# Optimization experiments

Hardware: AMD Instinct MI355X
Metric: run time of the kernel (lower is better)

The kernel has to match this reference:

```python
import jax, jax.numpy as jnp
import numpy as np

H = 28; W = 28; N = H * W
P = N              # padded max persistence pairs per homology dimension
T = 32             # landscape resolution
K1, K2 = 2, 3      # K_max for the two topo layers
M0_1, M0_2 = 0.05, 0.2
LIMS = ((1.0, 28.0), (1.0, 28.0))


def _make_nbrs(h, w, conn8):
    idx = np.arange(h * w).reshape(h, w)
    offs = [(-1, 0), (1, 0), (0, -1), (0, 1)]
    if conn8:
        offs += [(-1, -1), (-1, 1), (1, -1), (1, 1)]
    nbrs = []
    for i in range(h):
        for j in range(w):
            cur = [idx[i + a, j + b] for a, b in offs if 0 <= i + a < h and 0 <= j + b < w]
            nbrs.append(np.asarray(cur, np.int64))
    return nbrs

_NBR4 = _make_nbrs(H, W, False)
_NBR8 = _make_nbrs(H, W, True)


def _h0_pairs(vals, nbrs):
    # 0-dim persistence pairs of a vertex-valued sublevel filtration (union-find, elder rule)
    order = np.argsort(vals, kind="stable")
    pos = np.empty(N, np.int64); pos[order] = np.arange(N)
    parent = np.arange(N); birth = np.arange(N)
    added = np.zeros(N, bool)
    bi = np.zeros(P, np.int32); di = np.zeros(P, np.int32)
    k = 0
    def find(x):
        r = x
        while parent[r] != r: r = parent[r]
        while parent[x] != r: parent[x], x = r, parent[x]
        return r
    for v in order:
        added[v] = True
        for u in nbrs[v]:
            if not added[u]: continue
            ru, rv = find(u), find(v)
            if ru == rv: continue
            if pos[birth[ru]] <= pos[birth[rv]]:
                lb = birth[rv]; parent[rv] = ru
            else:
                lb = birth[ru]; parent[ru] = rv
            if k < P:
                bi[k] = lb; di[k] = v; k += 1
    return bi, di


def _pers_pairs_np(x):
    # x: [M, N] -> (birth_idx, death_idx) each [M, 2, P]; padded pairs point at idx 0 (zero persistence)
    x = np.asarray(x, np.float64)
    M = x.shape[0]
    bi = np.zeros((M, 2, P), np.int32); di = np.zeros((M, 2, P), np.int32)
    for m in range(M):
        b0, d0 = _h0_pairs(x[m], _NBR4)      # H0: sublevel, 4-connectivity
        b1, d1 = _h0_pairs(-x[m], _NBR8)     # H1 by Alexander duality: H0 of superlevel, 8-connectivity
        bi[m, 0], di[m, 0] = b0, d0
        bi[m, 1], di[m, 1] = d1, b1          # H1 birth = vals[d1], death = vals[b1]
    return bi, di


def _grid_d2():
    xs = np.linspace(LIMS[0][0], LIMS[0][1], H)
    ys = np.linspace(LIMS[1][0], LIMS[1][1], W)
    gx, gy = np.meshgrid(xs, ys, indexing="ij")
    pts = np.stack([gx.ravel(), gy.ravel()], 1)              # [N, 2] grid coordinates
    d2 = ((pts[:, None, :] - pts[None, :, :]) ** 2).sum(-1)  # [N, N] squared distances
    si = np.argsort(d2, axis=1, kind="stable")
    return jnp.asarray(si), jnp.asarray(np.take_along_axis(d2, si, 1), jnp.float32)

_SORT_IDX, _D2S = _grid_d2()


def dtm(x_flat, m0):
    # weighted distance-to-measure on the pixel grid, r=2; x_flat: [M, N] positive weights
    bound = m0 * jnp.sum(x_flat, -1, keepdims=True)                        # [M, 1]
    ws = x_flat[:, _SORT_IDX]                                              # [M, N, N] weights in distance order
    cum = jnp.cumsum(ws, -1)
    eff = jnp.minimum(jnp.maximum(bound[..., None] - (cum - ws), 0.0), ws) # effective mass per neighbor
    return jnp.sqrt(jnp.sum(eff * _D2S, -1) / bound)                       # [M, N]


def _landscape(vals, bi, di, start, end, K):
    # persistence landscape lambda_k sampled on T points from (birth, death) critical-vertex indices
    M = vals.shape[0]
    mi = jnp.arange(M)[:, None, None]
    b = vals[mi, bi]; d = vals[mi, di]                                     # [M, 2, P]
    t = jnp.linspace(start, end, T, dtype=vals.dtype)                      # [T]
    tent = jnp.maximum(jnp.minimum(t - b[..., None], d[..., None] - t), 0.0)  # [M, 2, P, T]
    lam, _ = jax.lax.top_k(jnp.swapaxes(tent, -1, -2), K)                  # [M, 2, T, K]
    return jnp.swapaxes(lam, -1, -2).reshape(M, 2 * K * T)                 # [M, dims*K*T]


def pl_features(vals, start, end, K):
    M = vals.shape[0]
    bi, di = jax.pure_callback(
        _pers_pairs_np,
        (jax.ShapeDtypeStruct((M, 2, P), np.int32),
         jax.ShapeDtypeStruct((M, 2, P), np.int32)),
        jax.lax.stop_gradient(vals))
    return _landscape(vals, bi, di, start, end, K)


def setup_inputs():
    key = jax.random.key(0)
    ks = jax.random.split(key, 7)
    B = 64
    return {
        "input": jax.random.uniform(ks[0], (B, 1, H, W), jnp.float32, 1e-3, 1.0),
        "w_g1": 0.1 * jax.random.normal(ks[1], (32, 2 * K1 * T), jnp.float32),
        "b_g1": 0.1 * jax.random.normal(ks[2], (32,), jnp.float32),
        "w_g2": 0.1 * jax.random.normal(ks[3], (32, 2 * K2 * T), jnp.float32),
        "b_g2": 0.1 * jax.random.normal(ks[4], (32,), jnp.float32),
        "w_fc": 0.1 * jax.random.normal(ks[5], (10, 64), jnp.float32),
        "b_fc": 0.1 * jax.random.normal(ks[6], (10,), jnp.float32),
    }


def reference(input, w_g1, b_g1, w_g2, b_g2, w_fc, b_fc):
    x_flat = input.reshape(-1, N)                                        # num_channels = 1
    f1 = dtm(x_flat, M0_1)
    f2 = dtm(x_flat, M0_2)
    x1 = jax.nn.relu(pl_features(f1, 0.0, 7.0, K1) @ w_g1.T + b_g1)      # topo layer 1 (start=0, end=7, K=2)
    x2 = jax.nn.relu(pl_features(f2, 1.0, 8.0, K2) @ w_g2.T + b_g2)      # topo layer 2 (start=1, end=8, K=3)
    return jnp.concatenate([x1, x2], -1) @ w_fc.T + b_fc                 # [B, num_classes]
```

## Files before the change

kernel.cpp:

```cpp
#include <hip/hip_runtime.h>

#define HW 28
#define NPIX 784
#define NIMG 64
#define MAXD2 1459
#define MAXREC 5504

#define DXPK 41048u
#define DYPK 34949u

__global__ void consts_sums_kernel(unsigned short* __restrict__ sortIdx,
                                   unsigned short* __restrict__ d2s,
                                   const float* __restrict__ x,
                                   float* __restrict__ sums) {
    int tid = threadIdx.x;
    if (blockIdx.x >= NPIX) {
        int m = blockIdx.x - NPIX;
        float acc = 0.f;
        for (int j = tid; j < NPIX; j += 256) acc += x[m * NPIX + j];
        for (int off = 32; off > 0; off >>= 1) acc += __shfl_down(acc, off, 64);
        __shared__ float red[4];
        int lane = tid & 63, w = tid >> 6;
        if (lane == 0) red[w] = acc;
        __syncthreads();
        if (tid == 0) sums[m] = red[0] + red[1] + red[2] + red[3];
        return;
    }
    __shared__ int cnt[MAXD2];
    __shared__ int d2v[NPIX];
    __shared__ int wtot[4];
    int i = blockIdx.x;
    for (int b = tid; b < MAXD2; b += 256) cnt[b] = 0;
    __syncthreads();
    int ii = i / HW, ij = i % HW;
    for (int j = tid; j < NPIX; j += 256) {
        int di = ii - j / HW, dj = ij - j % HW;
        int d = di * di + dj * dj;
        d2v[j] = d;
        atomicAdd(&cnt[d], 1);
    }
    __syncthreads();
    int b0 = tid * 6;
    int lc[6];
    int s0 = 0;
    #pragma unroll
    for (int t = 0; t < 6; ++t) {
        int b = b0 + t;
        lc[t] = (b < MAXD2) ? cnt[b] : 0;
        s0 += lc[t];
    }
    int lane = tid & 63, wv = tid >> 6;
    int v = s0;
    for (int off = 1; off < 64; off <<= 1) {
        int t2 = __shfl_up(v, off, 64);
        if (lane >= off) v += t2;
    }
    if (lane == 63) wtot[wv] = v;
    __syncthreads();
    int wadd = 0;
    for (int w2 = 0; w2 < wv; ++w2) wadd += wtot[w2];
    int run = wadd + v - s0;
    __syncthreads();
    #pragma unroll
    for (int t = 0; t < 6; ++t) {
        int b = b0 + t;
        if (b < MAXD2) { cnt[b] = run; run += lc[t]; }
    }
    __syncthreads();
    for (int j = tid; j < NPIX; j += 256) {
        int d = d2v[j];
        int slot = atomicAdd(&cnt[d], 1);
        sortIdx[i * NPIX + slot] = (unsigned short)j;
        d2s[i * NPIX + slot] = (unsigned short)d;
    }
}

__global__ void dtm_kernel(const float* __restrict__ x,
                           const unsigned short* __restrict__ sortIdx,
                           const unsigned short* __restrict__ d2s,
                           const float* __restrict__ sums,
                           float* __restrict__ F) {
    int wid = blockIdx.x * 4 + (threadIdx.x >> 6);
    int lane = threadIdx.x & 63;
    int m = wid / NPIX;
    int i = wid % NPIX;
    if (m >= NIMG) return;
    float s = sums[m];
    float bound1 = 0.05f * s, bound2 = 0.2f * s;
    const float* xr = x + m * NPIX;
    const unsigned short* si = sortIdx + (size_t)i * NPIX;
    const unsigned short* dr = d2s + (size_t)i * NPIX;
    float carry = 0.f, acc1 = 0.f, acc2 = 0.f;
    for (int c = 0; c < 4; ++c) {
        int j0 = c * 256 + lane * 4;
        float w0 = 0.f, w1 = 0.f, w2 = 0.f, w3 = 0.f;
        float d0 = 0.f, d1 = 0.f, d2 = 0.f, d3 = 0.f;
        if (j0 < NPIX) {
            ushort4 sv = *(const ushort4*)(si + j0);
            ushort4 dv = *(const ushort4*)(dr + j0);
            w0 = xr[sv.x]; w1 = xr[sv.y]; w2 = xr[sv.z]; w3 = xr[sv.w];
            d0 = (float)dv.x; d1 = (float)dv.y; d2 = (float)dv.z; d3 = (float)dv.w;
        }
        float ps = w0 + w1 + w2 + w3;
        float v = ps;
        for (int off = 1; off < 64; off <<= 1) {
            float t = __shfl_up(v, off, 64);
            if (lane >= off) v += t;
        }
        float c0 = carry + v - ps;
        float c1 = c0 + w0, c2 = c1 + w1, c3 = c2 + w2;
        acc1 += fminf(fmaxf(bound1 - c0, 0.f), w0) * d0
              + fminf(fmaxf(bound1 - c1, 0.f), w1) * d1
              + fminf(fmaxf(bound1 - c2, 0.f), w2) * d2
              + fminf(fmaxf(bound1 - c3, 0.f), w3) * d3;
        acc2 += fminf(fmaxf(bound2 - c0, 0.f), w0) * d0
              + fminf(fmaxf(bound2 - c1, 0.f), w1) * d1
              + fminf(fmaxf(bound2 - c2, 0.f), w2) * d2
              + fminf(fmaxf(bound2 - c3, 0.f), w3) * d3;
        carry += __shfl(v, 63, 64);
        if (carry >= bound2) break;
    }
    for (int off = 32; off > 0; off >>= 1) {
        acc1 += __shfl_down(acc1, off, 64);
        acc2 += __shfl_down(acc2, off, 64);
    }
    if (lane == 0) {
        F[0 * NIMG * NPIX + m * NPIX + i] = sqrtf(acc1 / bound1);
        F[1 * NIMG * NPIX + m * NPIX + i] = sqrtf(acc2 / bound2);
    }
}

template<int NN>
__device__ int uf_basin_run(const int* posA, const int* ordA,
                            int* bas, int* comp, int* recs, int* pairsI,
                            int2* mergeLDS, int* shInts, int* wtot4) {
    const int tid = threadIdx.x;
    const int lane = tid & 63, wv = tid >> 6;

    for (int s = tid; s < NPIX; s += 256) {
        int si = s / HW, sj = s % HW;
        int bestPos = posA[s], best = s;
        #pragma unroll
        for (int o = 0; o < NN; ++o) {
            int dx = ((DXPK >> (2 * o)) & 3) - 1;
            int dy = ((DYPK >> (2 * o)) & 3) - 1;
            int ui = si + dx, uj = sj + dy;
            if ((unsigned)ui < (unsigned)HW && (unsigned)uj < (unsigned)HW) {
                int u = ui * HW + uj;
                int pu = posA[u];
                if (pu < bestPos) { bestPos = pu; best = u; }
            }
        }
        bas[s] = best;
    }
    __syncthreads();

    for (int it = 0; it < 10; ++it) {
        int changed = 0;
        for (int s = tid; s < NPIX; s += 256) {
            int b = bas[s];
            int bb = bas[b];
            if (bb != b) { bas[s] = bb; changed = 1; }
        }
        if (__syncthreads_count(changed) == 0) break;
    }

    int nrec = 0;
    for (int c = 0; c < 4; ++c) {
        int r = c * 256 + tid;
        int cnt = 0;
        int myr[NN - 1];
        int got[NN - 1];
        #pragma unroll
        for (int t = 0; t < NN - 1; ++t) { got[t] = -1; myr[t] = 0; }
        if (r > 0 && r < NPIX) {
            int v = ordA[r];
            int vi = v / HW, vj = v % HW;
            int pivot = bas[v];
            #pragma unroll
            for (int o = 0; o < NN; ++o) {
                int dx = ((DXPK >> (2 * o)) & 3) - 1;
                int dy = ((DYPK >> (2 * o)) & 3) - 1;
                int ui = vi + dx, uj = vj + dy;
                if ((unsigned)ui < (unsigned)HW && (unsigned)uj < (unsigned)HW) {
                    int u = ui * HW + uj;
                    if (posA[u] < r) {
                        int b = bas[u];
                        bool dup = (b == pivot);
                        #pragma unroll
                        for (int t = 0; t < NN - 1; ++t) dup = dup || (got[t] == b);
                        if (!dup) {
                            #pragma unroll
                            for (int t = 0; t < NN - 1; ++t)
                                if (t == cnt) { got[t] = b; myr[t] = (v << 20) | (pivot << 10) | b; }
                            cnt++;
                        }
                    }
                }
            }
        }
        int p = cnt;
        for (int off = 1; off < 64; off <<= 1) {
            int t2 = __shfl_up(p, off, 64);
            if (lane >= off) p += t2;
        }
        if (lane == 63) wtot4[wv] = p;
        __syncthreads();
        int wadd = 0;
        for (int w2 = 0; w2 < wv; ++w2) wadd += wtot4[w2];
        int tot = wtot4[0] + wtot4[1] + wtot4[2] + wtot4[3];
        int excl = wadd + p - cnt;
        #pragma unroll
        for (int t = 0; t < NN - 1; ++t)
            if (t < cnt) recs[nrec + excl + t] = myr[t];
        nrec += tot;
        __syncthreads();
    }

    int k = 0;
    for (int base = 0; base < nrec; base += 64) {
        int nrem = 0;
        if (wv == 0) {
            int idx = base + lane;
            int rec = (idx < nrec) ? recs[idx] : 0;
            int pa = (rec >> 10) & 1023, pbn = rec & 1023;
            int ka = 0, kb = 0;
            if (idx < nrec) { ka = comp[pa]; kb = comp[pbn]; }
            for (;;) {
                unsigned long long d = __ballot(ka != kb);
                if (d == 0ull) break;
                int i = (int)__ffsll((long long)d) - 1;
                int sA = __builtin_amdgcn_readlane(ka, i);
                int sB = __builtin_amdgcn_readlane(kb, i);
                int w = min(sA, sB), l = max(sA, sB);
                int sv = __builtin_amdgcn_readlane(rec, i) >> 20;
                if (lane == 0) {
                    pairsI[k] = (l & 1023) | (sv << 10);
                    mergeLDS[nrem] = make_int2(l, w);
                }
                k++;
                ka = (ka == l) ? w : ka;
                kb = (kb == l) ? w : kb;
                nrem++;
                if (nrem == 63) {
                    for (int s = lane; s < NPIX; s += 64) {
                        int cv = comp[s], c0 = cv;
                        for (int e = 0; e < nrem; ++e) {
                            int2 me = mergeLDS[e];
                            cv = (cv == me.x) ? me.y : cv;
                        }
                        if (cv != c0) comp[s] = cv;
                    }
                    if (idx < nrec) { ka = comp[pa]; kb = comp[pbn]; }
                    nrem = 0;
                }
            }
            if (lane == 0) shInts[0] = nrem;
        }
        __syncthreads();
        int nr = shInts[0];
        if (nr > 0) {
            for (int s = tid; s < NPIX; s += 256) {
                int cv = comp[s], c0 = cv;
                for (int e = 0; e < nr; ++e) {
                    int2 me = mergeLDS[e];
                    cv = (cv == me.x) ? me.y : cv;
                }
                if (cv != c0) comp[s] = cv;
            }
        }
        __syncthreads();
    }
    if (tid == 0) shInts[1] = k;
    __syncthreads();
    return shInts[1];
}

__global__ void __launch_bounds__(256) uf_land_kernel(const float* __restrict__ F,
                                                      float* __restrict__ LAM1,
                                                      float* __restrict__ LAM2) {
    __shared__ int posA[NPIX], ordA[NPIX], bas[NPIX], comp[NPIX], pairsI[NPIX];
    __shared__ unsigned int ukey[NPIX];
    __shared__ float fv[NPIX];
    __shared__ float2 pairs[NPIX];
    __shared__ int recs[MAXREC];
    __shared__ int2 mergeLDS[64];
    __shared__ int shInts[2];
    __shared__ int wtot4[4];
    int tid = threadIdx.x;
    int task = blockIdx.x;
    int feat = task >> 7;
    int dir = (task >> 6) & 1;
    int m = task & 63;
    const float* fr = F + feat * NIMG * NPIX + m * NPIX;

    for (int j = tid; j < NPIX; j += 256) {
        float f = fr[j];
        fv[j] = f;
        unsigned int b = __float_as_uint(f);
        ukey[j] = dir ? ~b : b;
    }
    __syncthreads();

    {
        unsigned long long pki[4];
        int rank[4] = {0, 0, 0, 0};
        bool val[4];
        #pragma unroll
        for (int r = 0; r < 4; ++r) {
            int i = tid + 256 * r;
            val[r] = (i < NPIX);
            pki[r] = val[r] ? (((unsigned long long)ukey[i] << 10) | (unsigned)i) : 0ull;
        }
        const uint4* k4 = (const uint4*)ukey;
        for (int c = 0; c < NPIX / 4; ++c) {
            uint4 kv = k4[c];
            unsigned q = 4u * c;
            unsigned long long p0 = ((unsigned long long)kv.x << 10) | q;
            unsigned long long p1 = ((unsigned long long)kv.y << 10) | (q + 1);
            unsigned long long p2 = ((unsigned long long)kv.z << 10) | (q + 2);
            unsigned long long p3 = ((unsigned long long)kv.w << 10) | (q + 3);
            #pragma unroll
            for (int r = 0; r < 4; ++r) {
                rank[r] += (int)(p0 < pki[r]) + (int)(p1 < pki[r])
                         + (int)(p2 < pki[r]) + (int)(p3 < pki[r]);
            }
        }
        #pragma unroll
        for (int r = 0; r < 4; ++r) {
            if (val[r]) {
                int i = tid + 256 * r;
                posA[i] = rank[r];
                ordA[rank[r]] = i;
            }
        }
    }
    __syncthreads();
    for (int s = tid; s < NPIX; s += 256) comp[s] = (posA[s] << 10) | s;

    int k;
    if (dir == 0) k = uf_basin_run<4>(posA, ordA, bas, comp, recs, pairsI,
                                      mergeLDS, shInts, wtot4);
    else          k = uf_basin_run<8>(posA, ordA, bas, comp, recs, pairsI,
                                      mergeLDS, shInts, wtot4);

    for (int s = tid; s < k; s += 256) {
        int p = pairsI[s];
        float fb = fv[p & 1023], fd = fv[p >> 10];
        pairs[s] = dir ? make_float2(fd, fb) : make_float2(fb, fd);
    }
    __syncthreads();

    if (tid < 32) {
        int t = tid;
        float start = (feat == 0) ? 0.f : 1.f;
        float end   = (feat == 0) ? 7.f : 8.f;
        float tv = start + (end - start) * ((float)t / 31.f);
        float v0 = 0.f, v1 = 0.f, v2 = 0.f;
        for (int p = 0; p < k; ++p) {
            float2 bd = pairs[p];
            float tent = fmaxf(fminf(tv - bd.x, bd.y - tv), 0.f);
            if (tent > v0)      { v2 = v1; v1 = v0; v0 = tent; }
            else if (tent > v1) { v2 = v1; v1 = tent; }
            else if (tent > v2) { v2 = tent; }
        }
        if (feat == 0) {
            float* lam = LAM1 + m * 128 + dir * 64;
            lam[0 * 32 + t] = v0;
            lam[1 * 32 + t] = v1;
        } else {
            float* lam = LAM2 + m * 192 + dir * 96;
            lam[0 * 32 + t] = v0;
            lam[1 * 32 + t] = v1;
            lam[2 * 32 + t] = v2;
        }
    }
}

__global__ void mlp_kernel(const float* __restrict__ LAM1, const float* __restrict__ LAM2,
                           const float* __restrict__ w1, const float* __restrict__ b1,
                           const float* __restrict__ w2, const float* __restrict__ b2,
                           const float* __restrict__ wf, const float* __restrict__ bf,
                           float* __restrict__ out) {
    __shared__ float xc[64];
    int m = blockIdx.x;
    int n = threadIdx.x;
    if (n < 32) {
        float acc = b1[n];
        const float* l = LAM1 + m * 128;
        for (int c = 0; c < 128; ++c) acc += w1[n * 128 + c] * l[c];
        xc[n] = fmaxf(acc, 0.f);
    } else {
        int n2 = n - 32;
        float acc = b2[n2];
        const float* l = LAM2 + m * 192;
        for (int c = 0; c < 192; ++c) acc += w2[n2 * 192 + c] * l[c];
        xc[n] = fmaxf(acc, 0.f);
    }
    __syncthreads();
    if (n < 10) {
        float acc = bf[n];
        for (int c = 0; c < 64; ++c) acc += wf[n * 64 + c] * xc[c];
        out[m * 10 + n] = acc;
    }
}

extern "C" void kernel_launch(void* const* d_in, const int* in_sizes, int n_in,
                              void* d_out, int out_size, void* d_ws, size_t ws_size,
                              hipStream_t stream) {
    const float* x  = (const float*)d_in[0];
    const float* w1 = (const float*)d_in[1];
    const float* b1 = (const float*)d_in[2];
    const float* w2 = (const float*)d_in[3];
    const float* b2 = (const float*)d_in[4];
    const float* wf = (const float*)d_in[5];
    const float* bf = (const float*)d_in[6];
    float* out = (float*)d_out;

    char* ws = (char*)d_ws;
    size_t off = 0;
    unsigned short* SORT = (unsigned short*)(ws + off); off += (size_t)NPIX * NPIX * 2;
    unsigned short* D2S  = (unsigned short*)(ws + off); off += (size_t)NPIX * NPIX * 2;
    float* SUMS = (float*)(ws + off); off += 256;
    float* F    = (float*)(ws + off); off += (size_t)2 * NIMG * NPIX * 4;
    float* LAM1 = (float*)(ws + off); off += (size_t)NIMG * 128 * 4;
    float* LAM2 = (float*)(ws + off); off += (size_t)NIMG * 192 * 4;

    consts_sums_kernel<<<NPIX + NIMG, 256, 0, stream>>>(SORT, D2S, x, SUMS);
    dtm_kernel<<<(NIMG * NPIX) / 4, 256, 0, stream>>>(x, SORT, D2S, SUMS, F);
    uf_land_kernel<<<256, 256, 0, stream>>>(F, LAM1, LAM2);
    mlp_kernel<<<NIMG, 64, 0, stream>>>(LAM1, LAM2, w1, b1, w2, b2, wf, bf, out);
}
```

Measured before the change: 147.6 us.

## Fuse image sums into DTM, stage image in LDS, fold MLP into last landscape block

The per-image sum moves from the constants kernel into the DTM kernel. Each DTM block now loads its image into shared memory, reduces the sum there, and gathers pixel values from LDS rather than global memory. The union-find pass packs position and basin into one shared word to halve the neighbour lookups. The separate MLP kernel is replaced by a last-block-done atomic counter in the landscape kernel, which then runs the MLP serially in one block. This removes a launch and the global gathers, but adds a memset, redundant per-block image loads and sums, and a serialized tail on a single block.

```diff
diff --git a/kernel.cpp b/kernel.cpp
--- a/kernel.cpp
+++ b/kernel.cpp
@@ -3,33 +3,20 @@
 #define HW 28
 #define NPIX 784
 #define NIMG 64
+#define NIG  196
 #define MAXD2 1459
 #define MAXREC 5504
 
 #define DXPK 41048u
 #define DYPK 34949u
 
-__global__ void consts_sums_kernel(unsigned short* __restrict__ sortIdx,
-                                   unsigned short* __restrict__ d2s,
-                                   const float* __restrict__ x,
-                                   float* __restrict__ sums) {
-    int tid = threadIdx.x;
-    if (blockIdx.x >= NPIX) {
-        int m = blockIdx.x - NPIX;
-        float acc = 0.f;
-        for (int j = tid; j < NPIX; j += 256) acc += x[m * NPIX + j];
-        for (int off = 32; off > 0; off >>= 1) acc += __shfl_down(acc, off, 64);
-        __shared__ float red[4];
-        int lane = tid & 63, w = tid >> 6;
-        if (lane == 0) red[w] = acc;
-        __syncthreads();
-        if (tid == 0) sums[m] = red[0] + red[1] + red[2] + red[3];
-        return;
-    }
+__global__ void consts_kernel(unsigned short* __restrict__ sortIdx,
+                              unsigned short* __restrict__ d2s) {
     __shared__ int cnt[MAXD2];
     __shared__ int d2v[NPIX];
     __shared__ int wtot[4];
     int i = blockIdx.x;
+    int tid = threadIdx.x;
     for (int b = tid; b < MAXD2; b += 256) cnt[b] = 0;
     __syncthreads();
     int ii = i / HW, ij = i % HW;
@@ -78,16 +65,23 @@
 __global__ void dtm_kernel(const float* __restrict__ x,
                            const unsigned short* __restrict__ sortIdx,
                            const unsigned short* __restrict__ d2s,
-                           const float* __restrict__ sums,
                            float* __restrict__ F) {
-    int wid = blockIdx.x * 4 + (threadIdx.x >> 6);
-    int lane = threadIdx.x & 63;
-    int m = wid / NPIX;
-    int i = wid % NPIX;
-    if (m >= NIMG) return;
-    float s = sums[m];
+    __shared__ float xs[NPIX];
+    __shared__ float red[4];
+    int m = blockIdx.x / NIG;
+    int ig = blockIdx.x % NIG;
+    int tid = threadIdx.x;
+    int lane = tid & 63, wv = tid >> 6;
+    const float* xr = x + m * NPIX;
+    float part = 0.f;
+    for (int j = tid; j < NPIX; j += 256) { float vx = xr[j]; xs[j] = vx; part += vx; }
+    for (int off = 32; off > 0; off >>= 1) part += __shfl_down(part, off, 64);
+    if (lane == 0) red[wv] = part;
+    __syncthreads();
+    float s = red[0] + red[1] + red[2] + red[3];
+
+    int i = ig * 4 + wv;
     float bound1 = 0.05f * s, bound2 = 0.2f * s;
-    const float* xr = x + m * NPIX;
     const unsigned short* si = sortIdx + (size_t)i * NPIX;
     const unsigned short* dr = d2s + (size_t)i * NPIX;
     float carry = 0.f, acc1 = 0.f, acc2 = 0.f;
@@ -98,7 +92,7 @@
         if (j0 < NPIX) {
             ushort4 sv = *(const ushort4*)(si + j0);
             ushort4 dv = *(const ushort4*)(dr + j0);
-            w0 = xr[sv.x]; w1 = xr[sv.y]; w2 = xr[sv.z]; w3 = xr[sv.w];
+            w0 = xs[sv.x]; w1 = xs[sv.y]; w2 = xs[sv.z]; w3 = xs[sv.w];
             d0 = (float)dv.x; d1 = (float)dv.y; d2 = (float)dv.z; d3 = (float)dv.w;
         }
         float ps = w0 + w1 + w2 + w3;
@@ -132,7 +126,8 @@
 
 template<int NN>
 __device__ int uf_basin_run(const int* posA, const int* ordA,
-                            int* bas, int* comp, int* recs, int* pairsI,
+                            int* bas, unsigned int* pb, int* comp,
+                            int* recs, int* pairsI,
                             int2* mergeLDS, int* shInts, int* wtot4) {
     const int tid = threadIdx.x;
     const int lane = tid & 63, wv = tid >> 6;
@@ -165,6 +160,10 @@
         if (__syncthreads_count(changed) == 0) break;
     }
 
+    for (int s = tid; s < NPIX; s += 256)
+        pb[s] = ((unsigned)posA[s] << 10) | (unsigned)bas[s];
+    __syncthreads();
+
     int nrec = 0;
     for (int c = 0; c < 4; ++c) {
         int r = c * 256 + tid;
@@ -176,7 +175,7 @@
         if (r > 0 && r < NPIX) {
             int v = ordA[r];
             int vi = v / HW, vj = v % HW;
-            int pivot = bas[v];
+            int pivot = (int)(pb[v] & 1023u);
             #pragma unroll
             for (int o = 0; o < NN; ++o) {
                 int dx = ((DXPK >> (2 * o)) & 3) - 1;
@@ -184,8 +183,9 @@
                 int ui = vi + dx, uj = vj + dy;
                 if ((unsigned)ui < (unsigned)HW && (unsigned)uj < (unsigned)HW) {
                     int u = ui * HW + uj;
-                    if (posA[u] < r) {
-                        int b = bas[u];
+                    unsigned e = pb[u];
+                    if ((int)(e >> 10) < r) {
+                        int b = (int)(e & 1023u);
                         bool dup = (b == pivot);
                         #pragma unroll
                         for (int t = 0; t < NN - 1; ++t) dup = dup || (got[t] == b);
@@ -278,15 +278,24 @@
 
 __global__ void __launch_bounds__(256) uf_land_kernel(const float* __restrict__ F,
                                                       float* __restrict__ LAM1,
-                                                      float* __restrict__ LAM2) {
+                                                      float* __restrict__ LAM2,
+                                                      const float* __restrict__ w1,
+                                                      const float* __restrict__ b1,
+                                                      const float* __restrict__ w2,
+                                                      const float* __restrict__ b2,
+                                                      const float* __restrict__ wf,
+                                                      const float* __restrict__ bf,
+                                                      float* __restrict__ out,
+                                                      int* __restrict__ cnt) {
     __shared__ int posA[NPIX], ordA[NPIX], bas[NPIX], comp[NPIX], pairsI[NPIX];
     __shared__ unsigned int ukey[NPIX];
     __shared__ float fv[NPIX];
     __shared__ float2 pairs[NPIX];
     __shared__ int recs[MAXREC];
     __shared__ int2 mergeLDS[64];
-    __shared__ int shInts[2];
+    __shared__ int shInts[3];
     __shared__ int wtot4[4];
+    __shared__ float xc[4][64];
     int tid = threadIdx.x;
     int task = blockIdx.x;
     int feat = task >> 7;
@@ -339,9 +348,9 @@
     for (int s = tid; s < NPIX; s += 256) comp[s] = (posA[s] << 10) | s;
 
     int k;
-    if (dir == 0) k = uf_basin_run<4>(posA, ordA, bas, comp, recs, pairsI,
+    if (dir == 0) k = uf_basin_run<4>(posA, ordA, bas, ukey, comp, recs, pairsI,
                                       mergeLDS, shInts, wtot4);
-    else          k = uf_basin_run<8>(posA, ordA, bas, comp, recs, pairsI,
+    else          k = uf_basin_run<8>(posA, ordA, bas, ukey, comp, recs, pairsI,
                                       mergeLDS, shInts, wtot4);
 
     for (int s = tid; s < k; s += 256) {
@@ -375,33 +384,36 @@
             lam[2 * 32 + t] = v2;
         }
     }
-}
-
-__global__ void mlp_kernel(const float* __restrict__ LAM1, const float* __restrict__ LAM2,
-                           const float* __restrict__ w1, const float* __restrict__ b1,
-                           const float* __restrict__ w2, const float* __restrict__ b2,
-                           const float* __restrict__ wf, const float* __restrict__ bf,
-                           float* __restrict__ out) {
-    __shared__ float xc[64];
-    int m = blockIdx.x;
-    int n = threadIdx.x;
-    if (n < 32) {
-        float acc = b1[n];
-        const float* l = LAM1 + m * 128;
-        for (int c = 0; c < 128; ++c) acc += w1[n * 128 + c] * l[c];
-        xc[n] = fmaxf(acc, 0.f);
-    } else {
-        int n2 = n - 32;
-        float acc = b2[n2];
-        const float* l = LAM2 + m * 192;
-        for (int c = 0; c < 192; ++c) acc += w2[n2 * 192 + c] * l[c];
-        xc[n] = fmaxf(acc, 0.f);
-    }
-    __syncthreads();
-    if (n < 10) {
-        float acc = bf[n];
-        for (int c = 0; c < 64; ++c) acc += wf[n * 64 + c] * xc[c];
-        out[m * 10 + n] = acc;
+
+    __threadfence();
+    __syncthreads();
+    if (tid == 0) shInts[2] = (atomicAdd(cnt, 1) == gridDim.x - 1);
+    __syncthreads();
+    if (shInts[2]) {
+        __threadfence();
+        int g = tid >> 6, n = tid & 63;
+        for (int pass = 0; pass < 16; ++pass) {
+            int mm = pass * 4 + g;
+            float acc;
+            if (n < 32) {
+                acc = b1[n];
+                const float* l = LAM1 + mm * 128;
+                for (int c = 0; c < 128; ++c) acc += w1[n * 128 + c] * l[c];
+            } else {
+                int n2 = n - 32;
+                acc = b2[n2];
+                const float* l = LAM2 + mm * 192;
+                for (int c = 0; c < 192; ++c) acc += w2[n2 * 192 + c] * l[c];
+            }
+            xc[g][n] = fmaxf(acc, 0.f);
+            __syncthreads();
+            if (n < 10) {
+                float o = bf[n];
+                for (int c = 0; c < 64; ++c) o += wf[n * 64 + c] * xc[g][c];
+                out[mm * 10 + n] = o;
+            }
+            __syncthreads();
+        }
     }
 }
 
@@ -421,13 +433,14 @@
     size_t off = 0;
     unsigned short* SORT = (unsigned short*)(ws + off); off += (size_t)NPIX * NPIX * 2;
     unsigned short* D2S  = (unsigned short*)(ws + off); off += (size_t)NPIX * NPIX * 2;
-    float* SUMS = (float*)(ws + off); off += 256;
     float* F    = (float*)(ws + off); off += (size_t)2 * NIMG * NPIX * 4;
     float* LAM1 = (float*)(ws + off); off += (size_t)NIMG * 128 * 4;
     float* LAM2 = (float*)(ws + off); off += (size_t)NIMG * 192 * 4;
-
-    consts_sums_kernel<<<NPIX + NIMG, 256, 0, stream>>>(SORT, D2S, x, SUMS);
-    dtm_kernel<<<(NIMG * NPIX) / 4, 256, 0, stream>>>(x, SORT, D2S, SUMS, F);
-    uf_land_kernel<<<256, 256, 0, stream>>>(F, LAM1, LAM2);
-    mlp_kernel<<<NIMG, 64, 0, stream>>>(LAM1, LAM2, w1, b1, w2, b2, wf, bf, out);
+    int* CNT    = (int*)(ws + off);   off += 256;
+
+    hipMemsetAsync(CNT, 0, 4, stream);
+    consts_kernel<<<NPIX, 256, 0, stream>>>(SORT, D2S);
+    dtm_kernel<<<NIMG * NIG, 256, 0, stream>>>(x, SORT, D2S, F);
+    uf_land_kernel<<<256, 256, 0, stream>>>(F, LAM1, LAM2,
+                                            w1, b1, w2, b2, wf, bf, out, CNT);
 }
```

New measurement: 286.5 us. 94.1% more time.
